# Kernel tuning notes

Hardware: AMD Instinct MI355X
Metric: run time of the kernel (lower is better)

Reference implementation:

```python
import jax, jax.numpy as jnp
import numpy as np

BASE = 10000.0

def _rope(x):
    # x: [b, n, h, d]; positions along token axis n, rotate-half convention
    d = x.shape[-1]
    n = x.shape[1]
    inv_freq = 1.0 / (BASE ** (jnp.arange(0, d, 2, dtype=jnp.float32) / d))  # [d/2]
    t = jnp.arange(n, dtype=jnp.float32)
    freqs = jnp.outer(t, inv_freq)                       # [n, d/2]
    emb = jnp.concatenate([freqs, freqs], axis=-1)       # [n, d]
    cos = jnp.cos(emb)[None, :, None, :]
    sin = jnp.sin(emb)[None, :, None, :]
    x1, x2 = jnp.split(x, 2, axis=-1)
    rot = jnp.concatenate([-x2, x1], axis=-1)
    return x * cos + rot * sin


def setup_inputs() -> dict:
    key = jax.random.key(0)
    k1, k2, k3 = jax.random.split(key, 3)
    b, c, hh, ww = 64, 1024, 16, 16
    x = jax.random.normal(k1, (b, c, hh, ww), dtype=jnp.float32)
    w_qkv = jax.random.normal(k2, (3 * c, c), dtype=jnp.float32) * 0.02
    w_lin = jax.random.normal(k3, (c, c, 1, 1), dtype=jnp.float32) * 0.02
    b_lin = jnp.zeros((c,), dtype=jnp.float32)
    return {"x": x, "w_qkv": w_qkv, "w_lin": w_lin, "b_lin": b_lin, "n_heads": 16}


def reference(x, w_qkv, w_lin, b_lin, n_heads):
    b, c, hh, ww = x.shape
    n = hh * ww
    d_head = c // n_heads
    scale = d_head ** -0.5
    # flatten(2).transpose(-2,-1): [b, n, c]
    xt = jnp.transpose(x.reshape(b, c, n), (0, 2, 1))
    # qkv proj, unflatten to [b, n, heads, 3*d_head], chunk along last dim
    qkv = (xt @ w_qkv.T).reshape(b, n, n_heads, 3 * d_head)
    q, k, v = jnp.split(qkv, 3, axis=-1)                  # each [b, n, h, d]
    q = _rope(q)
    k = _rope(k)
    q = jax.nn.softmax(q, axis=-1) * scale                # softmax over d_head
    k = jax.nn.softmax(k, axis=-2)                        # softmax over heads axis (as in torch code)
    # k^T @ v over the heads axis -> per-token [d_head, d_head] context
    context = jnp.einsum('bnhd,bnhe->bnde', k, v)
    o = jnp.einsum('bnhd,bnde->bnhe', q, context)         # [b, n, h, d]
    # transpose(-2,-1).reshape(b, c, h, w)
    o = jnp.transpose(o, (0, 1, 3, 2)).reshape(b, c, hh, ww)
    # 1x1 conv
    return jnp.einsum('bchw,oc->bohw', o, w_lin[:, :, 0, 0]) + b_lin[None, :, None, None]
```

## Files before the change

kernel.cpp:

```cpp
#include <hip/hip_runtime.h>
#include <hip/hip_bf16.h>
#include <math.h>

typedef __hip_bfloat16 hbf16;
typedef __attribute__((ext_vector_type(8))) __bf16    bf16x8;
typedef __attribute__((ext_vector_type(4))) float     f32x4;
typedef __attribute__((ext_vector_type(4))) _Float16  f16x4;

#define C_    1024
#define NTOK  256
#define NH    16
#define J3    3072

__device__ __forceinline__ float b2f(hbf16 v){ return __bfloat162float(v); }
__device__ __forceinline__ unsigned short fbits(float v){
    return __builtin_bit_cast(unsigned short, __float2bfloat16(v));
}
__device__ __forceinline__ __bf16 to_bf(float v){
    return __builtin_bit_cast(__bf16, __float2bfloat16(v));
}

__device__ __forceinline__ void gload_lds16(const __bf16* g, __bf16* l) {
    __builtin_amdgcn_global_load_lds((const __attribute__((address_space(1))) void*)g,
                                     (__attribute__((address_space(3))) void*)l, 16, 0, 0);
}

__global__ __launch_bounds__(256) void cvt_bf16(const float* __restrict__ in,
                                                __bf16* __restrict__ out, int n4) {
    int i = blockIdx.x * 256 + threadIdx.x;
    if (i < n4) {
        float4 v = ((const float4*)in)[i];
        ushort4 u;
        u.x = fbits(v.x); u.y = fbits(v.y); u.z = fbits(v.z); u.w = fbits(v.w);
        ((ushort4*)out)[i] = u;
    }
}

__global__ __launch_bounds__(256) void xpose_x(const float* __restrict__ X,
                                               __bf16* __restrict__ Xt) {
    __shared__ float t[32][36];
    const int b = blockIdx.z, k0 = blockIdx.y * 32, s0 = blockIdx.x * 32;
    const int tid = threadIdx.x;
    {
        int kl = tid >> 3, s4 = (tid & 7) * 4;
        float4 v = *(const float4*)(X + ((size_t)b << 18) + (size_t)(k0 + kl) * 256 + s0 + s4);
        t[kl][s4] = v.x; t[kl][s4 + 1] = v.y; t[kl][s4 + 2] = v.z; t[kl][s4 + 3] = v.w;
    }
    __syncthreads();
    {
        int sl = tid >> 3, k4 = (tid & 7) * 4;
        ushort4 u;
        u.x = fbits(t[k4][sl]); u.y = fbits(t[k4 + 1][sl]);
        u.z = fbits(t[k4 + 2][sl]); u.w = fbits(t[k4 + 3][sl]);
        *(ushort4*)(Xt + (size_t)(b * 256 + s0 + sl) * 1024 + k0 + k4) = u;
    }
}

template <int EPI>
__global__ __launch_bounds__(256) void mfma_gemm(const __bf16* __restrict__ A,
                                                 const __bf16* __restrict__ B,
                                                 void* __restrict__ Cout,
                                                 const float* __restrict__ bias) {
    __shared__ union __align__(16) {
        struct { __bf16 A[128 * 64]; __bf16 B[128 * 64]; } kl;
        __bf16 stY[128][136];
        float  stO[128][68];
    } sm;

    const int tid  = threadIdx.x;
    const int wave = tid >> 6, lane = tid & 63;
    const int wm = wave & 1, wn = wave >> 1;
    const int m0 = blockIdx.x * 128, n0 = blockIdx.y * 128;

    const int srow = lane >> 3;
    const int lchunk = (lane & 7) ^ srow;

    f32x4 acc[4][4] = {};

    for (int kk = 0; kk < 1024; kk += 64) {
        #pragma unroll
        for (int g4 = 0; g4 < 4; ++g4) {
            const int g = g4 * 4 + wave;
            const int row = g * 8 + srow;
            gload_lds16(A + (((size_t)(m0 + row)) << 10) + kk + lchunk * 8,
                        &sm.kl.A[g * 512]);
            gload_lds16(B + (((size_t)(n0 + row)) << 10) + kk + lchunk * 8,
                        &sm.kl.B[g * 512]);
        }
        __syncthreads();

        #pragma unroll
        for (int t = 0; t < 2; ++t) {
            const int chunk = t * 4 + (lane >> 4);
            bf16x8 af[4], bf[4];
            #pragma unroll
            for (int mi = 0; mi < 4; ++mi) {
                int row = wm * 64 + mi * 16 + (lane & 15);
                af[mi] = *(const bf16x8*)&sm.kl.A[row * 64 + ((chunk ^ (row & 7)) << 3)];
            }
            #pragma unroll
            for (int ni = 0; ni < 4; ++ni) {
                int row = wn * 64 + ni * 16 + (lane & 15);
                bf[ni] = *(const bf16x8*)&sm.kl.B[row * 64 + ((chunk ^ (row & 7)) << 3)];
            }
            #pragma unroll
            for (int mi = 0; mi < 4; ++mi)
                #pragma unroll
                for (int ni = 0; ni < 4; ++ni)
                    acc[mi][ni] = __builtin_amdgcn_mfma_f32_16x16x32_bf16(
                        af[mi], bf[ni], acc[mi][ni], 0, 0, 0);
        }
        __syncthreads();
    }

    const int cl = lane & 15, rq = lane >> 4;

    if (EPI == 0) {
        __syncthreads();
        #pragma unroll
        for (int mi = 0; mi < 4; ++mi)
            #pragma unroll
            for (int ni = 0; ni < 4; ++ni) {
                int row = wm * 64 + mi * 16 + rq * 4;
                int col = wn * 64 + ni * 16 + cl;
                #pragma unroll
                for (int j = 0; j < 4; ++j)
                    sm.stY[row + j][col] = to_bf(acc[mi][ni][j]);
            }
        __syncthreads();
        __bf16* Y = (__bf16*)Cout;
        #pragma unroll
        for (int i = 0; i < 8; ++i) {
            int cid = tid + 256 * i;
            int r = cid >> 4, c8 = (cid & 15) * 8;
            *(bf16x8*)(Y + (size_t)(m0 + r) * 3072 + n0 + c8) =
                *(const bf16x8*)&sm.stY[r][c8];
        }
    } else {
        float* out = (float*)Cout;
        const int bb = m0 >> 8;
        const int sbase = m0 & 255;
        #pragma unroll
        for (int p = 0; p < 2; ++p) {
            __syncthreads();
            if (wm == p) {
                #pragma unroll
                for (int mi = 0; mi < 4; ++mi)
                    #pragma unroll
                    for (int ni = 0; ni < 4; ++ni) {
                        int rloc = mi * 16 + rq * 4;
                        int col  = wn * 64 + ni * 16 + cl;
                        *(f32x4*)&sm.stO[col][rloc] = acc[mi][ni];
                    }
            }
            __syncthreads();
            #pragma unroll
            for (int i = 0; i < 8; ++i) {
                int cid = tid + 256 * i;
                int ocl = cid >> 4, d4 = (cid & 15) * 4;
                f32x4 v = *(const f32x4*)&sm.stO[ocl][d4];
                float bv = bias[n0 + ocl];
                v += bv;
                *(f32x4*)(out + ((size_t)bb << 18) + ((size_t)(n0 + ocl) << 8)
                          + sbase + p * 64 + d4) = v;
            }
        }
    }
}

__global__ __launch_bounds__(256) void attn_mfma(const __bf16* __restrict__ Y,
                                                 __bf16* __restrict__ Ot) {
    __shared__ __bf16 vst[4][1024];

    const int tid  = threadIdx.x;
    const int wave = tid >> 6, lane = tid & 63;
    const int token = blockIdx.x * 4 + wave;
    const int b = token >> 8, n = token & 255;
    const int quad = lane >> 4, m = lane & 15;
    const __bf16* Yt = Y + (size_t)token * J3;

    #pragma unroll
    for (int p = 0; p < 2; ++p) {
        const int h = p * 8 + (lane >> 3), part = lane & 7;
        gload_lds16(Yt + h * 192 + 128 + part * 8, &vst[wave][p * 512]);
    }

    bf16x8 qb[2], kb[2];
    #pragma unroll
    for (int st = 0; st < 2; ++st) {
        qb[st] = *(const bf16x8*)(Yt + m * 192 +      st * 32 + quad * 8);
        kb[st] = *(const bf16x8*)(Yt + m * 192 + 64 + st * 32 + quad * 8);
    }
    float qf[16], kf[16];
    #pragma unroll
    for (int st = 0; st < 2; ++st)
        #pragma unroll
        for (int j = 0; j < 8; ++j) {
            qf[st * 8 + j] = (float)qb[st][j];
            kf[st * 8 + j] = (float)kb[st][j];
        }

    const float fn = (float)n;
    #pragma unroll
    for (int j = 0; j < 8; ++j) {
        const float d  = (float)(quad * 8 + j);
        const float th = fn * __expf(-0.28782313662425572f * d);
        const float sn = __sinf(th), cn = __cosf(th);
        float a0 = qf[j], a1 = qf[8 + j];
        qf[j]     = a0 * cn - a1 * sn;
        qf[8 + j] = a1 * cn + a0 * sn;
        float b0 = kf[j], b1 = kf[8 + j];
        kf[j]     = b0 * cn - b1 * sn;
        kf[8 + j] = b1 * cn + b0 * sn;
    }

    float qe[16], ls = 0.f;
    #pragma unroll
    for (int i = 0; i < 16; ++i) { qe[i] = __expf(qf[i]); ls += qe[i]; }
    ls += __shfl_xor(ls, 16);
    ls += __shfl_xor(ls, 32);
    const float qinv = 0.125f * __builtin_amdgcn_rcpf(ls);
    bf16x8 qbh[2];
    #pragma unroll
    for (int st = 0; st < 2; ++st)
        #pragma unroll
        for (int j = 0; j < 8; ++j) qbh[st][j] = to_bf(qe[st * 8 + j] * qinv);

    float ke[16], kc[16];
    #pragma unroll
    for (int i = 0; i < 16; ++i) { ke[i] = __expf(kf[i]); kc[i] = ke[i]; }
    #pragma unroll
    for (int msk = 1; msk <= 8; msk <<= 1)
        #pragma unroll
        for (int i = 0; i < 16; ++i) kc[i] += __shfl_xor(kc[i], msk);
    bf16x8 kbh[2];
    #pragma unroll
    for (int st = 0; st < 2; ++st)
        #pragma unroll
        for (int j = 0; j < 8; ++j)
            kbh[st][j] = to_bf(ke[st * 8 + j] * __builtin_amdgcn_rcpf(kc[st * 8 + j]));

    f32x4 Sp = {0.f, 0.f, 0.f, 0.f};
    Sp = __builtin_amdgcn_mfma_f32_16x16x32_bf16(kbh[0], qbh[0], Sp, 0, 0, 0);
    Sp = __builtin_amdgcn_mfma_f32_16x16x32_bf16(kbh[1], qbh[1], Sp, 0, 0, 0);

    __syncthreads();

#if __has_builtin(__builtin_amdgcn_mfma_f32_16x16x16f16)
    f16x4 af;
    #pragma unroll
    for (int r = 0; r < 4; ++r) af[r] = (_Float16)Sp[r];
    f32x4 o4[4];
    #pragma unroll
    for (int tile = 0; tile < 4; ++tile) {
        f16x4 bv;
        #pragma unroll
        for (int j = 0; j < 4; ++j)
            bv[j] = (_Float16)(float)vst[wave][(quad * 4 + j) * 64 + tile * 16 + m];
        f32x4 z = {0.f, 0.f, 0.f, 0.f};
        o4[tile] = __builtin_amdgcn_mfma_f32_16x16x16f16(af, bv, z, 0, 0, 0);
    }
#else
    bf16x8 a2;
    #pragma unroll
    for (int j = 0; j < 8; ++j) {
        int k = quad * 8 + j;
        int src = ((k & 15) >> 2) * 16 + m;
        float v = __shfl(Sp[k & 3], src, 64);
        a2[j] = (quad < 2) ? to_bf(v) : to_bf(0.f);
    }
    f32x4 o4[4];
    #pragma unroll
    for (int tile = 0; tile < 4; ++tile) {
        bf16x8 bv;
        #pragma unroll
        for (int j = 0; j < 8; ++j) {
            int k = quad * 8 + j;
            int kk = (k < 16) ? k : 0;
            bv[j] = vst[wave][kk * 64 + tile * 16 + m];
        }
        f32x4 z = {0.f, 0.f, 0.f, 0.f};
        o4[tile] = __builtin_amdgcn_mfma_f32_16x16x32_bf16(a2, bv, z, 0, 0, 0);
    }
#endif

    __bf16* Ob = Ot + (((size_t)(b * 256)) << 10) + n * 4;
    #pragma unroll
    for (int r = 0; r < 4; ++r) {
        const int sth = m * 16 + quad * 4 + r;
        ushort4 u;
        u.x = fbits(o4[0][r]); u.y = fbits(o4[1][r]);
        u.z = fbits(o4[2][r]); u.w = fbits(o4[3][r]);
        *(ushort4*)(Ob + ((size_t)sth << 10)) = u;
    }
}

extern "C" void kernel_launch(void* const* d_in, const int* in_sizes, int n_in,
                              void* d_out, int out_size, void* d_ws, size_t ws_size,
                              hipStream_t stream) {
    const float* x     = (const float*)d_in[0];
    const float* w_qkv = (const float*)d_in[1];
    const float* w_lin = (const float*)d_in[2];
    const float* b_lin = (const float*)d_in[3];
    float* out = (float*)d_out;

    char* ws = (char*)d_ws;
    __bf16* Y    = (__bf16*)ws;
    __bf16* XtOt = (__bf16*)(ws + (size_t)100663296);
    __bf16* Wqb  = (__bf16*)(ws + (size_t)134217728);
    __bf16* Wlb  = (__bf16*)(ws + (size_t)140509184);

    cvt_bf16<<<3072, 256, 0, stream>>>(w_qkv, Wqb, 786432);
    cvt_bf16<<<1024, 256, 0, stream>>>(w_lin, Wlb, 262144);
    xpose_x<<<dim3(8, 32, 64), 256, 0, stream>>>(x, XtOt);

    mfma_gemm<0><<<dim3(128, 24), 256, 0, stream>>>(XtOt, Wqb, (void*)Y, nullptr);
    attn_mfma<<<4096, 256, 0, stream>>>(Y, XtOt);
    mfma_gemm<1><<<dim3(128, 8), 256, 0, stream>>>(XtOt, Wlb, (void*)out, b_lin);
}
```

Measured before the change: 345.6 us.

## Coalesce attention output via LDS staging, swap GEMM operands, merge weight casts

The attention kernel now runs 16 tokens per 1024-thread block and stages its outputs in a swizzled LDS buffer. Each row of the transposed output is then written as contiguous 32-byte stores instead of scattered 8-byte writes. The final projection GEMM swaps its operands so the weight is the M side, letting the epilogue write the NCHW output directly from registers without the LDS transpose. This relies on per-lane scalar stores being reasonably coalesced. The two weight conversion kernels are merged into one launch.

```diff
diff --git a/kernel.cpp b/kernel.cpp
--- a/kernel.cpp
+++ b/kernel.cpp
@@ -6,13 +6,13 @@
 typedef __attribute__((ext_vector_type(8))) __bf16    bf16x8;
 typedef __attribute__((ext_vector_type(4))) float     f32x4;
 typedef __attribute__((ext_vector_type(4))) _Float16  f16x4;
+typedef __attribute__((ext_vector_type(8))) unsigned short u16x8;
 
 #define C_    1024
 #define NTOK  256
 #define NH    16
 #define J3    3072
 
-__device__ __forceinline__ float b2f(hbf16 v){ return __bfloat162float(v); }
 __device__ __forceinline__ unsigned short fbits(float v){
     return __builtin_bit_cast(unsigned short, __float2bfloat16(v));
 }
@@ -25,15 +25,17 @@
                                      (__attribute__((address_space(3))) void*)l, 16, 0, 0);
 }
 
-__global__ __launch_bounds__(256) void cvt_bf16(const float* __restrict__ in,
-                                                __bf16* __restrict__ out, int n4) {
-    int i = blockIdx.x * 256 + threadIdx.x;
-    if (i < n4) {
-        float4 v = ((const float4*)in)[i];
-        ushort4 u;
-        u.x = fbits(v.x); u.y = fbits(v.y); u.z = fbits(v.z); u.w = fbits(v.w);
-        ((ushort4*)out)[i] = u;
-    }
+__global__ __launch_bounds__(256) void cvt_w(const float* __restrict__ wq,
+                                             __bf16* __restrict__ wqo,
+                                             const float* __restrict__ wl,
+                                             __bf16* __restrict__ wlo) {
+    const float* in; __bf16* out; int i;
+    if (blockIdx.x < 3072) { in = wq; out = wqo; i = blockIdx.x * 256 + threadIdx.x; }
+    else                   { in = wl; out = wlo; i = (blockIdx.x - 3072) * 256 + threadIdx.x; }
+    float4 v = ((const float4*)in)[i];
+    ushort4 u;
+    u.x = fbits(v.x); u.y = fbits(v.y); u.z = fbits(v.z); u.w = fbits(v.w);
+    ((ushort4*)out)[i] = u;
 }
 
 __global__ __launch_bounds__(256) void xpose_x(const float* __restrict__ X,
@@ -64,7 +66,6 @@
     __shared__ union __align__(16) {
         struct { __bf16 A[128 * 64]; __bf16 B[128 * 64]; } kl;
         __bf16 stY[128][136];
-        float  stO[128][68];
     } sm;
 
     const int tid  = threadIdx.x;
@@ -138,51 +139,47 @@
         }
     } else {
         float* out = (float*)Cout;
-        const int bb = m0 >> 8;
-        const int sbase = m0 & 255;
-        #pragma unroll
-        for (int p = 0; p < 2; ++p) {
-            __syncthreads();
-            if (wm == p) {
+        float bia[4][4];
+        const int rbase = m0 + wm * 64 + rq * 4;
+        #pragma unroll
+        for (int mi = 0; mi < 4; ++mi)
+            #pragma unroll
+            for (int j = 0; j < 4; ++j) bia[mi][j] = bias[rbase + mi * 16 + j];
+        const int nbase = n0 + wn * 64 + cl;
+        #pragma unroll
+        for (int mi = 0; mi < 4; ++mi)
+            #pragma unroll
+            for (int ni = 0; ni < 4; ++ni) {
+                int nn = nbase + ni * 16;
+                size_t base = ((size_t)(nn >> 8) << 18) + (nn & 255);
                 #pragma unroll
-                for (int mi = 0; mi < 4; ++mi)
-                    #pragma unroll
-                    for (int ni = 0; ni < 4; ++ni) {
-                        int rloc = mi * 16 + rq * 4;
-                        int col  = wn * 64 + ni * 16 + cl;
-                        *(f32x4*)&sm.stO[col][rloc] = acc[mi][ni];
-                    }
+                for (int j = 0; j < 4; ++j) {
+                    int oc = rbase + mi * 16 + j;
+                    out[base + ((size_t)oc << 8)] = acc[mi][ni][j] + bia[mi][j];
+                }
             }
-            __syncthreads();
-            #pragma unroll
-            for (int i = 0; i < 8; ++i) {
-                int cid = tid + 256 * i;
-                int ocl = cid >> 4, d4 = (cid & 15) * 4;
-                f32x4 v = *(const f32x4*)&sm.stO[ocl][d4];
-                float bv = bias[n0 + ocl];
-                v += bv;
-                *(f32x4*)(out + ((size_t)bb << 18) + ((size_t)(n0 + ocl) << 8)
-                          + sbase + p * 64 + d4) = v;
-            }
-        }
-    }
-}
-
-__global__ __launch_bounds__(256) void attn_mfma(const __bf16* __restrict__ Y,
-                                                 __bf16* __restrict__ Ot) {
-    __shared__ __bf16 vst[4][1024];
+    }
+}
+
+__global__ __launch_bounds__(1024) void attn_mfma(const __bf16* __restrict__ Y,
+                                                  __bf16* __restrict__ Ot) {
+    __shared__ union __align__(16) {
+        __bf16  v[16][1024];
+        ushort4 ost[256][16];
+    } sm;
 
     const int tid  = threadIdx.x;
     const int wave = tid >> 6, lane = tid & 63;
-    const int token = blockIdx.x * 4 + wave;
-    const int b = token >> 8, n = token & 255;
+    const int bb = blockIdx.x >> 4;
+    const int n0 = (blockIdx.x & 15) * 16;
+    const int n  = n0 + wave;
     const int quad = lane >> 4, m = lane & 15;
-    const __bf16* Yt = Y + (size_t)token * J3;
+    const __bf16* Yt = Y + (size_t)(bb * 256 + n) * J3;
 
     #pragma unroll
     for (int p = 0; p < 2; ++p) {
         const int h = p * 8 + (lane >> 3), part = lane & 7;
-        gload_lds16(Yt + h * 192 + 128 + part * 8, &vst[wave][p * 512]);
+        gload_lds16(Yt + h * 192 + 128 + part * 8, &sm.v[wave][p * 512]);
     }
 
     bf16x8 qb[2], kb[2];
@@ -246,17 +243,17 @@
 
     __syncthreads();
 
+    f32x4 o4[4];
 #if __has_builtin(__builtin_amdgcn_mfma_f32_16x16x16f16)
     f16x4 af;
     #pragma unroll
     for (int r = 0; r < 4; ++r) af[r] = (_Float16)Sp[r];
-    f32x4 o4[4];
     #pragma unroll
     for (int tile = 0; tile < 4; ++tile) {
         f16x4 bv;
         #pragma unroll
         for (int j = 0; j < 4; ++j)
-            bv[j] = (_Float16)(float)vst[wave][(quad * 4 + j) * 64 + tile * 16 + m];
+            bv[j] = (_Float16)(float)sm.v[wave][(quad * 4 + j) * 64 + tile * 16 + m];
         f32x4 z = {0.f, 0.f, 0.f, 0.f};
         o4[tile] = __builtin_amdgcn_mfma_f32_16x16x16f16(af, bv, z, 0, 0, 0);
     }
@@ -269,7 +266,6 @@
         float v = __shfl(Sp[k & 3], src, 64);
         a2[j] = (quad < 2) ? to_bf(v) : to_bf(0.f);
     }
-    f32x4 o4[4];
     #pragma unroll
     for (int tile = 0; tile < 4; ++tile) {
         bf16x8 bv;
@@ -277,21 +273,40 @@
         for (int j = 0; j < 8; ++j) {
             int k = quad * 8 + j;
             int kk = (k < 16) ? k : 0;
-            bv[j] = vst[wave][kk * 64 + tile * 16 + m];
+            bv[j] = sm.v[wave][kk * 64 + tile * 16 + m];
         }
         f32x4 z = {0.f, 0.f, 0.f, 0.f};
         o4[tile] = __builtin_amdgcn_mfma_f32_16x16x32_bf16(a2, bv, z, 0, 0, 0);
     }
 #endif
 
-    __bf16* Ob = Ot + (((size_t)(b * 256)) << 10) + n * 4;
+    __syncthreads();
+
     #pragma unroll
     for (int r = 0; r < 4; ++r) {
-        const int sth = m * 16 + quad * 4 + r;
+        const int s = m * 16 + quad * 4 + r;
+        const int phys = wave ^ (quad * 4 + r) ^ m;
         ushort4 u;
         u.x = fbits(o4[0][r]); u.y = fbits(o4[1][r]);
         u.z = fbits(o4[2][r]); u.w = fbits(o4[3][r]);
-        *(ushort4*)(Ob + ((size_t)sth << 10)) = u;
+        sm.ost[s][phys] = u;
+    }
+    __syncthreads();
+
+    {
+        const int row = tid >> 2;
+        const int w0  = (tid & 3) * 4;
+        ushort4 u4[4];
+        #pragma unroll
+        for (int j = 0; j < 4; ++j) {
+            const int phys = (w0 + j) ^ (row & 15) ^ (row >> 4);
+            u4[j] = sm.ost[row][phys];
+        }
+        __bf16* dst = Ot + (((size_t)(bb * 256 + row)) << 10) + n0 * 4 + w0 * 4;
+        u16x8 a = {u4[0].x, u4[0].y, u4[0].z, u4[0].w, u4[1].x, u4[1].y, u4[1].z, u4[1].w};
+        u16x8 b = {u4[2].x, u4[2].y, u4[2].z, u4[2].w, u4[3].x, u4[3].y, u4[3].z, u4[3].w};
+        *(u16x8*)dst = a;
+        *(u16x8*)(dst + 8) = b;
     }
 }
 
@@ -310,11 +325,10 @@
     __bf16* Wqb  = (__bf16*)(ws + (size_t)134217728);
     __bf16* Wlb  = (__bf16*)(ws + (size_t)140509184);
 
-    cvt_bf16<<<3072, 256, 0, stream>>>(w_qkv, Wqb, 786432);
-    cvt_bf16<<<1024, 256, 0, stream>>>(w_lin, Wlb, 262144);
+    cvt_w<<<4096, 256, 0, stream>>>(w_qkv, Wqb, w_lin, Wlb);
     xpose_x<<<dim3(8, 32, 64), 256, 0, stream>>>(x, XtOt);
 
     mfma_gemm<0><<<dim3(128, 24), 256, 0, stream>>>(XtOt, Wqb, (void*)Y, nullptr);
-    attn_mfma<<<4096, 256, 0, stream>>>(Y, XtOt);
-    mfma_gemm<1><<<dim3(128, 8), 256, 0, stream>>>(XtOt, Wlb, (void*)out, b_lin);
-}
+    attn_mfma<<<1024, 1024, 0, stream>>>(Y, XtOt);
+    mfma_gemm<1><<<dim3(8, 128), 256, 0, stream>>>(Wlb, XtOt, (void*)out, b_lin);
+}
```

After: 335.0 us. 1.03x faster.
